# Kernel tuning notes

Measured on AMD Instinct MI355X. Metric: run time of the kernel, lower is better.

The kernel has to match this reference:

```python
import jax, jax.numpy as jnp
import numpy as np

B, N, J, D = 16384, 4096, 256, 9  # batch, input_dim, output_dim, ultimate_depth


def _rotate(state, angle):
    # state: [J, N], angle: [J]
    # Circulant gate: out[i] = cos*v[i] - sin*v[(i+1)%N] + sin*v[(i-1)%N]
    c = jnp.cos(angle)[:, None]
    s = jnp.sin(angle)[:, None]
    return c * state - s * jnp.roll(state, -1, axis=1) + s * jnp.roll(state, 1, axis=1)


def setup_inputs() -> dict:
    key = jax.random.key(0)
    k0, k1, k2, k3 = jax.random.split(key, 4)
    return {
        "x": jax.random.normal(k0, (B, N), dtype=jnp.float32),
        "ultimate_weights": jax.random.normal(k1, (D, N, J), dtype=jnp.float32),
        "classical_weights": jax.random.normal(k2, (N, J), dtype=jnp.float32),
        "classical_biases": jax.random.normal(k3, (J,), dtype=jnp.float32),
    }


def reference(x, ultimate_weights, classical_weights, classical_biases):
    batch = x.shape[0]
    depth, n_in, _ = ultimate_weights.shape
    n_out = classical_weights.shape[1]

    classical = x @ classical_weights + classical_biases  # [B, J]

    # Ultimate processing: batch-independent; vectorized over output dim j.
    state = jnp.ones((n_out, n_in), dtype=x.dtype) / jnp.sqrt(
        jnp.asarray(n_in, dtype=x.dtype)
    )  # [J, N]
    angles = ultimate_weights[:, :n_out, :3]  # [D, J, 3]

    def step(st, ang):  # ang: [J, 3] -> consciousness, intelligence, wisdom gates
        st = _rotate(st, ang[:, 0])
        st = _rotate(st, ang[:, 1])
        st = _rotate(st, ang[:, 2])
        return st, None

    state, _ = jax.lax.scan(step, state, angles)
    prob = jnp.abs(state[:, 0]) ** 2  # [J]
    ultimate = jnp.broadcast_to(prob, (batch, n_out))

    return jnp.tanh(classical + ultimate)
```

## Files before the change

kernel.cpp:

```cpp
#include <hip/hip_runtime.h>
#include <math.h>

#define K_DIM 4096
#define N_DIM 256
#define M_DIM 16384
#define NSTAGES 128
#define ABUF 4096

typedef short bf8v __attribute__((ext_vector_type(8)));
typedef float f32x16 __attribute__((ext_vector_type(16)));
typedef unsigned short us8 __attribute__((ext_vector_type(8)));

union AB { unsigned u[4]; bf8v v; };

__device__ __forceinline__ unsigned cvt_pk(float a, float b) {
    unsigned r;
    asm("v_cvt_pk_bf16_f32 %0, %1, %2" : "=v"(r) : "v"(a), "v"(b));
    return r;
}

__global__ void beta_kernel(const float* __restrict__ uw,
                            const float* __restrict__ bias,
                            float* __restrict__ beta) {
    int j = threadIdx.x;
    float p = 1.0f / 4096.0f;
    #pragma unroll
    for (int d = 0; d < 9; ++d) {
        const float* a = uw + (size_t)d * (K_DIM * N_DIM) + (size_t)j * N_DIM;
        #pragma unroll
        for (int k = 0; k < 3; ++k) {
            float c = cosf(a[k]);
            p *= c * c;
        }
    }
    beta[j] = bias[j] + p;
}

__global__ void pretile_w_kernel(const float* __restrict__ W,
                                 unsigned short* __restrict__ Bt) {
    const int s = blockIdx.x;
    const int t = threadIdx.x;
    #pragma unroll
    for (int g = 0; g < 8; ++g) {
        const int G  = g * 256 + t;
        const int w  = G >> 8;
        const int h  = (G >> 7) & 1;
        const int ks = (G >> 6) & 1;
        const int l  = G & 63;
        const int n  = w * 32 + (l & 31);
        const int k0 = s * 32 + ks * 16 + (l >> 5) * 8;
        unsigned short o8[8];
        #pragma unroll
        for (int j = 0; j < 8; ++j) {
            float f = W[(size_t)(k0 + j) * N_DIM + n];
            unsigned u = __float_as_uint(f);
            unsigned hh = u + 0x7fffu + ((u >> 16) & 1u);
            if (h == 0) {
                o8[j] = (unsigned short)(hh >> 16);
            } else {
                float r = f - __uint_as_float(hh & 0xffff0000u);
                unsigned ur = __float_as_uint(r);
                o8[j] = (unsigned short)((ur + 0x7fffu + ((ur >> 16) & 1u)) >> 16);
            }
        }
        *(us8*)&Bt[((size_t)s * 2048 + G) * 8] = *(us8*)&o8[0];
    }
}

__global__ __launch_bounds__(512, 4)
void gemm_tanh_kernel(const float* __restrict__ X,
                      const unsigned short* __restrict__ Bt,
                      const float* __restrict__ beta,
                      float* __restrict__ out) {
    __shared__ __align__(16) char lds[2 * ABUF];

    const int t = threadIdx.x;
    const int lane = t & 63;
    const int w = t >> 6;
    const int l31 = lane & 31;
    const int lh = lane >> 5;
    const int m0 = blockIdx.x * 32;

    const int srow = t >> 4;
    const int kp = t & 15;
    const float* pa = X + (size_t)(m0 + srow) * K_DIM + kp * 2;
    const int whi_off = srow * 128 + ((((kp >> 2)    ) ^ (srow & 7)) << 4) + (kp & 3) * 4;
    const int wlo_off = srow * 128 + ((((kp >> 2) + 4) ^ (srow & 7)) << 4) + (kp & 3) * 4;

    const int fx = (l31 & 7) << 4;
    const int rb = l31 * 128;
    const int ro_h0 = rb + (((0 + lh) << 4) ^ fx);
    const int ro_h1 = rb + (((2 + lh) << 4) ^ fx);
    const int ro_l0 = rb + (((4 + lh) << 4) ^ fx);
    const int ro_l1 = rb + (((6 + lh) << 4) ^ fx);

    const unsigned short* pb = Bt + w * 2048 + lane * 8;

    f32x16 acc = (f32x16)(0.0f);
    float2 araw;
    AB bA[4], bB[4];

#define LOADB(dst, sidx) { \
    const unsigned short* p_ = pb + (size_t)(sidx) * 16384; \
    dst[0].v = *(const bf8v*)(p_);           \
    dst[1].v = *(const bf8v*)(p_ + 512);     \
    dst[2].v = *(const bf8v*)(p_ + 1024);    \
    dst[3].v = *(const bf8v*)(p_ + 1536); }

#define CVTWR(ar, NB) { \
    unsigned hp_ = cvt_pk(ar.x, ar.y); \
    float r0_ = ar.x - __uint_as_float(hp_ << 16);           \
    float r1_ = ar.y - __uint_as_float(hp_ & 0xffff0000u); \
    unsigned lp_ = cvt_pk(r0_, r1_); \
    *(unsigned*)(lds + (NB) + whi_off) = hp_; \
    *(unsigned*)(lds + (NB) + wlo_off) = lp_; }

#define MFMA(a, b) acc = __builtin_amdgcn_mfma_f32_32x32x16_bf16((a), (b), acc, 0, 0, 0)

    {
        float2 a0 = *(const float2*)pa;
        CVTWR(a0, 0);
        araw = *(const float2*)(pa + 32);
        LOADB(bA, 0);
        asm volatile("s_waitcnt lgkmcnt(0)\n\ts_barrier" ::: "memory");
    }

#define BODY(s, CB, NB, BCUR, BNXT) { \
    CVTWR(araw, NB); \
    araw = *(const float2*)(pa + (size_t)(((s) + 2) & 127) * 32); \
    LOADB(BNXT, ((s) + 1) & 127); \
    AB ah0, ah1, al0, al1; \
    ah0.v = *(const bf8v*)(lds + (CB) + ro_h0); \
    ah1.v = *(const bf8v*)(lds + (CB) + ro_h1); \
    al0.v = *(const bf8v*)(lds + (CB) + ro_l0); \
    al1.v = *(const bf8v*)(lds + (CB) + ro_l1); \
    MFMA(ah0.v, BCUR[0].v); \
    MFMA(al0.v, BCUR[0].v); \
    MFMA(ah0.v, BCUR[2].v); \
    MFMA(ah1.v, BCUR[1].v); \
    MFMA(al1.v, BCUR[1].v); \
    MFMA(ah1.v, BCUR[3].v); \
    asm volatile("s_waitcnt lgkmcnt(0)\n\ts_barrier" ::: "memory"); \
}

    for (int s = 0; s < NSTAGES; s += 2) {
        BODY(s,     0,    ABUF, bA, bB);
        BODY(s + 1, ABUF, 0,    bB, bA);
    }

#undef BODY
#undef MFMA
#undef CVTWR
#undef LOADB

    const float bet = beta[w * 32 + l31];
    float* po = out + (size_t)(m0 + 4 * lh) * N_DIM + w * 32 + l31;
    #pragma unroll
    for (int r = 0; r < 16; ++r) {
        const int row = (r & 3) + 8 * (r >> 2);
        po[(size_t)row * N_DIM] = tanhf(acc[r] + bet);
    }
}

extern "C" void kernel_launch(void* const* d_in, const int* in_sizes, int n_in,
                              void* d_out, int out_size, void* d_ws, size_t ws_size,
                              hipStream_t stream) {
    const float* x    = (const float*)d_in[0];
    const float* uw   = (const float*)d_in[1];
    const float* W    = (const float*)d_in[2];
    const float* bias = (const float*)d_in[3];
    float* out = (float*)d_out;

    char* ws = (char*)d_ws;
    unsigned short* bt = (unsigned short*)ws;
    float* beta = (float*)(ws + (size_t)4 * 1024 * 1024);

    pretile_w_kernel<<<dim3(NSTAGES), 256, 0, stream>>>(W, bt);
    beta_kernel<<<1, 256, 0, stream>>>(uw, bias, beta);

    gemm_tanh_kernel<<<dim3(M_DIM / 32), 512, 0, stream>>>(x, bt, beta, out);
}
```

Baseline: 540.0 us.

## Drop LDS staging and have each wave load and split its own A tile

The GEMM no longer stages A through shared memory with a barrier every stage. Each wave now reads its own 32 rows of X straight from global memory into registers, splits them into bf16 hi/lo in registers, and computes one 32x32 output tile on a 2D grid of N-blocks by M-blocks. The goal is to remove the per-stage LDS round trip and barrier stalls. In exchange, each X tile is now read and converted once per N-block, so there is more global or L2 traffic, more redundant conversion work, and strided per-lane loads. The beta computation is also folded into the pretile kernel as an extra block to save a launch.

```diff
diff --git a/kernel.cpp b/kernel.cpp
--- a/kernel.cpp
+++ b/kernel.cpp
@@ -5,7 +5,6 @@
 #define N_DIM 256
 #define M_DIM 16384
 #define NSTAGES 128
-#define ABUF 4096
 
 typedef short bf8v __attribute__((ext_vector_type(8)));
 typedef float f32x16 __attribute__((ext_vector_type(16)));
@@ -19,27 +18,27 @@
     return r;
 }
 
-__global__ void beta_kernel(const float* __restrict__ uw,
-                            const float* __restrict__ bias,
-                            float* __restrict__ beta) {
-    int j = threadIdx.x;
-    float p = 1.0f / 4096.0f;
-    #pragma unroll
-    for (int d = 0; d < 9; ++d) {
-        const float* a = uw + (size_t)d * (K_DIM * N_DIM) + (size_t)j * N_DIM;
+__global__ void pretile_w_kernel(const float* __restrict__ W,
+                                 unsigned short* __restrict__ Bt,
+                                 const float* __restrict__ uw,
+                                 const float* __restrict__ bias,
+                                 float* __restrict__ beta) {
+    const int t = threadIdx.x;
+    if (blockIdx.x == NSTAGES) {
+        float p = 1.0f / 4096.0f;
         #pragma unroll
-        for (int k = 0; k < 3; ++k) {
-            float c = cosf(a[k]);
-            p *= c * c;
+        for (int d = 0; d < 9; ++d) {
+            const float* a = uw + (size_t)d * (K_DIM * N_DIM) + (size_t)t * N_DIM;
+            #pragma unroll
+            for (int k = 0; k < 3; ++k) {
+                float c = cosf(a[k]);
+                p *= c * c;
+            }
         }
+        beta[t] = bias[t] + p;
+        return;
     }
-    beta[j] = bias[j] + p;
-}
-
-__global__ void pretile_w_kernel(const float* __restrict__ W,
-                                 unsigned short* __restrict__ Bt) {
     const int s = blockIdx.x;
-    const int t = threadIdx.x;
     #pragma unroll
     for (int g = 0; g < 8; ++g) {
         const int G  = g * 256 + t;
@@ -67,94 +66,87 @@
     }
 }
 
-__global__ __launch_bounds__(512, 4)
+__global__ __launch_bounds__(256, 4)
 void gemm_tanh_kernel(const float* __restrict__ X,
                       const unsigned short* __restrict__ Bt,
                       const float* __restrict__ beta,
                       float* __restrict__ out) {
-    __shared__ __align__(16) char lds[2 * ABUF];
-
     const int t = threadIdx.x;
     const int lane = t & 63;
     const int w = t >> 6;
     const int l31 = lane & 31;
     const int lh = lane >> 5;
-    const int m0 = blockIdx.x * 32;
+    const int bn = blockIdx.x;
+    const int mrow = blockIdx.y * 128 + w * 32 + l31;
 
-    const int srow = t >> 4;
-    const int kp = t & 15;
-    const float* pa = X + (size_t)(m0 + srow) * K_DIM + kp * 2;
-    const int whi_off = srow * 128 + ((((kp >> 2)    ) ^ (srow & 7)) << 4) + (kp & 3) * 4;
-    const int wlo_off = srow * 128 + ((((kp >> 2) + 4) ^ (srow & 7)) << 4) + (kp & 3) * 4;
-
-    const int fx = (l31 & 7) << 4;
-    const int rb = l31 * 128;
-    const int ro_h0 = rb + (((0 + lh) << 4) ^ fx);
-    const int ro_h1 = rb + (((2 + lh) << 4) ^ fx);
-    const int ro_l0 = rb + (((4 + lh) << 4) ^ fx);
-    const int ro_l1 = rb + (((6 + lh) << 4) ^ fx);
-
-    const unsigned short* pb = Bt + w * 2048 + lane * 8;
+    const float* pa = X + (size_t)mrow * K_DIM + lh * 8;
+    const unsigned short* pb = Bt + bn * 2048 + lane * 8;
 
     f32x16 acc = (f32x16)(0.0f);
-    float2 araw;
-    AB bA[4], bB[4];
+    float4 a0_0, a0_1, a0_2, a0_3;
+    float4 a1_0, a1_1, a1_2, a1_3;
+    AB b0_0, b0_1, b0_2, b0_3;
+    AB b1_0, b1_1, b1_2, b1_3;
 
-#define LOADB(dst, sidx) { \
+#define LOADA(P, sidx) { \
+    const float* p_ = pa + (size_t)(sidx) * 32; \
+    a##P##_0 = *(const float4*)(p_);      \
+    a##P##_1 = *(const float4*)(p_ + 4);  \
+    a##P##_2 = *(const float4*)(p_ + 16); \
+    a##P##_3 = *(const float4*)(p_ + 20); }
+
+#define LOADB(P, sidx) { \
     const unsigned short* p_ = pb + (size_t)(sidx) * 16384; \
-    dst[0].v = *(const bf8v*)(p_);           \
-    dst[1].v = *(const bf8v*)(p_ + 512);     \
-    dst[2].v = *(const bf8v*)(p_ + 1024);    \
-    dst[3].v = *(const bf8v*)(p_ + 1536); }
+    b##P##_0.v = *(const bf8v*)(p_);        \
+    b##P##_1.v = *(const bf8v*)(p_ + 512);  \
+    b##P##_2.v = *(const bf8v*)(p_ + 1024); \
+    b##P##_3.v = *(const bf8v*)(p_ + 1536); }
 
-#define CVTWR(ar, NB) { \
-    unsigned hp_ = cvt_pk(ar.x, ar.y); \
-    float r0_ = ar.x - __uint_as_float(hp_ << 16);           \
-    float r1_ = ar.y - __uint_as_float(hp_ & 0xffff0000u); \
-    unsigned lp_ = cvt_pk(r0_, r1_); \
-    *(unsigned*)(lds + (NB) + whi_off) = hp_; \
-    *(unsigned*)(lds + (NB) + wlo_off) = lp_; }
+#define CVT8(f0, f1, hi, lo) { \
+    float x0_ = f0.x, x1_ = f0.y, x2_ = f0.z, x3_ = f0.w; \
+    float x4_ = f1.x, x5_ = f1.y, x6_ = f1.z, x7_ = f1.w; \
+    unsigned h0_ = cvt_pk(x0_, x1_); \
+    unsigned h1_ = cvt_pk(x2_, x3_); \
+    unsigned h2_ = cvt_pk(x4_, x5_); \
+    unsigned h3_ = cvt_pk(x6_, x7_); \
+    hi.u[0] = h0_; hi.u[1] = h1_; hi.u[2] = h2_; hi.u[3] = h3_; \
+    lo.u[0] = cvt_pk(x0_ - __uint_as_float(h0_ << 16), x1_ - __uint_as_float(h0_ & 0xffff0000u)); \
+    lo.u[1] = cvt_pk(x2_ - __uint_as_float(h1_ << 16), x3_ - __uint_as_float(h1_ & 0xffff0000u)); \
+    lo.u[2] = cvt_pk(x4_ - __uint_as_float(h2_ << 16), x5_ - __uint_as_float(h2_ & 0xffff0000u)); \
+    lo.u[3] = cvt_pk(x6_ - __uint_as_float(h3_ << 16), x7_ - __uint_as_float(h3_ & 0xffff0000u)); }
 
 #define MFMA(a, b) acc = __builtin_amdgcn_mfma_f32_32x32x16_bf16((a), (b), acc, 0, 0, 0)
 
-    {
-        float2 a0 = *(const float2*)pa;
-        CVTWR(a0, 0);
-        araw = *(const float2*)(pa + 32);
-        LOADB(bA, 0);
-        asm volatile("s_waitcnt lgkmcnt(0)\n\ts_barrier" ::: "memory");
-    }
-
-#define BODY(s, CB, NB, BCUR, BNXT) { \
-    CVTWR(araw, NB); \
-    araw = *(const float2*)(pa + (size_t)(((s) + 2) & 127) * 32); \
-    LOADB(BNXT, ((s) + 1) & 127); \
-    AB ah0, ah1, al0, al1; \
-    ah0.v = *(const bf8v*)(lds + (CB) + ro_h0); \
-    ah1.v = *(const bf8v*)(lds + (CB) + ro_h1); \
-    al0.v = *(const bf8v*)(lds + (CB) + ro_l0); \
-    al1.v = *(const bf8v*)(lds + (CB) + ro_l1); \
-    MFMA(ah0.v, BCUR[0].v); \
-    MFMA(al0.v, BCUR[0].v); \
-    MFMA(ah0.v, BCUR[2].v); \
-    MFMA(ah1.v, BCUR[1].v); \
-    MFMA(al1.v, BCUR[1].v); \
-    MFMA(ah1.v, BCUR[3].v); \
-    asm volatile("s_waitcnt lgkmcnt(0)\n\ts_barrier" ::: "memory"); \
+#define BODY(P, s) { \
+    AB ah0_, al0_, ah1_, al1_; \
+    CVT8(a##P##_0, a##P##_1, ah0_, al0_); \
+    CVT8(a##P##_2, a##P##_3, ah1_, al1_); \
+    LOADA(P, ((s) + 2) & 127); \
+    MFMA(ah0_.v, b##P##_0.v); \
+    MFMA(al0_.v, b##P##_0.v); \
+    MFMA(ah0_.v, b##P##_2.v); \
+    MFMA(ah1_.v, b##P##_1.v); \
+    MFMA(al1_.v, b##P##_1.v); \
+    MFMA(ah1_.v, b##P##_3.v); \
+    LOADB(P, ((s) + 2) & 127); \
 }
 
+    LOADA(0, 0); LOADA(1, 1);
+    LOADB(0, 0); LOADB(1, 1);
+
     for (int s = 0; s < NSTAGES; s += 2) {
-        BODY(s,     0,    ABUF, bA, bB);
-        BODY(s + 1, ABUF, 0,    bB, bA);
+        BODY(0, s);
+        BODY(1, s + 1);
     }
 
 #undef BODY
 #undef MFMA
-#undef CVTWR
+#undef CVT8
 #undef LOADB
+#undef LOADA
 
-    const float bet = beta[w * 32 + l31];
-    float* po = out + (size_t)(m0 + 4 * lh) * N_DIM + w * 32 + l31;
+    const float bet = beta[bn * 32 + l31];
+    float* po = out + (size_t)(blockIdx.y * 128 + w * 32 + 4 * lh) * N_DIM + bn * 32 + l31;
     #pragma unroll
     for (int r = 0; r < 16; ++r) {
         const int row = (r & 3) + 8 * (r >> 2);
@@ -175,8 +167,7 @@
     unsigned short* bt = (unsigned short*)ws;
     float* beta = (float*)(ws + (size_t)4 * 1024 * 1024);
 
-    pretile_w_kernel<<<dim3(NSTAGES), 256, 0, stream>>>(W, bt);
-    beta_kernel<<<1, 256, 0, stream>>>(uw, bias, beta);
+    pretile_w_kernel<<<dim3(NSTAGES + 1), 256, 0, stream>>>(W, bt, uw, bias, beta);
 
-    gemm_tanh_kernel<<<dim3(M_DIM / 32), 512, 0, stream>>>(x, bt, beta, out);
+    gemm_tanh_kernel<<<dim3(N_DIM / 32, M_DIM / 128), 256, 0, stream>>>(x, bt, beta, out);
 }
```

Result: slower. 962.9 us (+78.3%).
